# Kernel tuning notes

Hardware: AMD Instinct MI355X
Metric: run time of the kernel (lower is better)

The kernel has to match this reference:

```python
import jax, jax.numpy as jnp
import numpy as np
import math

B, T, D = 2, 2048, 1024
H, NL, DF = 16, 6, 4096
HD = D // H
EPS = 1e-5

def layer_norm(x, w, b):
    mu = jnp.mean(x, axis=-1, keepdims=True)
    var = jnp.mean((x - mu) ** 2, axis=-1, keepdims=True)
    return (x - mu) * jax.lax.rsqrt(var + EPS) * w + b

def setup_inputs() -> dict:
    key = jax.random.key(0)
    ks = jax.random.split(key, 12)
    def w(k, shape, scale=0.02):
        return jax.random.normal(k, shape, dtype=jnp.float32) * scale
    inp = {
        'sequences': jax.random.normal(ks[0], (B, T, D), dtype=jnp.float32),
        'Wq': w(ks[1], (NL, D, D)), 'bq': jnp.zeros((NL, D), jnp.float32),
        'Wk': w(ks[2], (NL, D, D)), 'bk': jnp.zeros((NL, D), jnp.float32),
        'Wv': w(ks[3], (NL, D, D)), 'bv': jnp.zeros((NL, D), jnp.float32),
        'Wo': w(ks[4], (NL, D, D)), 'bo': jnp.zeros((NL, D), jnp.float32),
        'Wz': w(ks[5], (NL, D, D)), 'bz': jnp.zeros((NL, D), jnp.float32),
        'Wr': w(ks[6], (NL, D, D)), 'br': jnp.zeros((NL, D), jnp.float32),
        'W1': w(ks[7], (NL, D, DF)), 'b1': jnp.zeros((NL, DF), jnp.float32),
        'W2': w(ks[8], (NL, DF, D)), 'b2': jnp.zeros((NL, D), jnp.float32),
        'ln1_w': jnp.ones((NL, D), jnp.float32), 'ln1_b': jnp.zeros((NL, D), jnp.float32),
        'ln2_w': jnp.ones((NL, D), jnp.float32), 'ln2_b': jnp.zeros((NL, D), jnp.float32),
        'lnf_w': jnp.ones((D,), jnp.float32), 'lnf_b': jnp.zeros((D,), jnp.float32),
    }
    return inp

def reference(sequences, Wq, bq, Wk, bk, Wv, bv, Wo, bo, Wz, bz, Wr, br,
              W1, b1, W2, b2, ln1_w, ln1_b, ln2_w, ln2_b, lnf_w, lnf_b):
    scale = 1.0 / math.sqrt(HD)
    causal = jnp.tril(jnp.ones((T, T), dtype=bool))  # mask[L:L+T, :L+T] with L=0
    x = sequences
    src = x
    for i in range(NL):
        xn = layer_norm(x, ln1_w[i], ln1_b[i])
        # QKV -> [B, H, T, HD]
        q = (xn @ Wq[i] + bq[i]).reshape(B, T, H, HD).transpose(0, 2, 1, 3)
        k = (xn @ Wk[i] + bk[i]).reshape(B, T, H, HD).transpose(0, 2, 1, 3)
        v = (xn @ Wv[i] + bv[i]).reshape(B, T, H, HD).transpose(0, 2, 1, 3)
        att = jnp.einsum('bhqd,bhkd->bhqk', q, k) * scale
        att = jnp.where(causal, att, -jnp.inf)
        att = jax.nn.softmax(att, axis=-1)
        y = jnp.einsum('bhqk,bhkd->bhqd', att, v)
        y = y.transpose(0, 2, 1, 3).reshape(B, T, D)
        x_attn = y @ Wo[i] + bo[i]
        z = jax.nn.sigmoid(xn @ Wz[i] + bz[i])
        r = jax.nn.sigmoid(xn @ Wr[i] + br[i])
        h_tilde = jnp.tanh(r * x_attn)
        x = (1.0 - z) * x + z * h_tilde
        xm = layer_norm(x, ln2_w[i], ln2_b[i])
        mlp = jax.nn.gelu(xm @ W1[i] + b1[i], approximate=False) @ W2[i] + b2[i]
        x = (1.0 - z) * x + z * mlp
        x = x + src
    x = layer_norm(x, lnf_w, lnf_b)
    return x
```

## Files before the change

### kernel.cpp

```cpp
#include <hip/hip_runtime.h>
#include <hip/hip_bf16.h>
#include <math.h>

#define B_ 2
#define T_ 2048
#define D_ 1024
#define H_ 16
#define NL_ 6
#define DF_ 4096
#define HD_ 64
#define M_ (B_*T_)

typedef __bf16 bf16;
typedef __attribute__((ext_vector_type(8))) __bf16 bf16x8;
typedef __attribute__((ext_vector_type(4))) float f32x4;
typedef __attribute__((ext_vector_type(16))) float f32x16;
typedef __attribute__((ext_vector_type(4))) unsigned u32x4;

#define BAR() __builtin_amdgcn_s_barrier()
#define LGKM0() asm volatile("s_waitcnt lgkmcnt(0)" ::: "memory")
#define VMC(n) asm volatile("s_waitcnt vmcnt(" #n ")" ::: "memory")

__device__ __forceinline__ void gload_lds16(const void* g, void* l) {
    __builtin_amdgcn_global_load_lds((const __attribute__((address_space(1))) void*)g,
                                     (__attribute__((address_space(3))) void*)l, 16, 0, 0);
}

__device__ __forceinline__ unsigned pk2(float a, float b) {
    bf16 lo = (bf16)a, hb = (bf16)b;
    return (unsigned)__builtin_bit_cast(unsigned short, lo) |
           ((unsigned)__builtin_bit_cast(unsigned short, hb) << 16);
}

template<bool OUT_BF16>
__global__ __launch_bounds__(256) void ln_kernel(const float* __restrict__ x,
        const float* __restrict__ w, const float* __restrict__ b,
        void* __restrict__ out) {
    const int row = blockIdx.x;
    const int t = threadIdx.x;
    const float4 xv = *(const float4*)(x + (long)row * D_ + t * 4);
    float s  = xv.x + xv.y + xv.z + xv.w;
    float sq = xv.x*xv.x + xv.y*xv.y + xv.z*xv.z + xv.w*xv.w;
    #pragma unroll
    for (int m = 32; m; m >>= 1) { s += __shfl_xor(s, m); sq += __shfl_xor(sq, m); }
    __shared__ float red[8];
    const int wid = t >> 6, lid = t & 63;
    if (lid == 0) { red[wid] = s; red[wid + 4] = sq; }
    __syncthreads();
    s  = red[0] + red[1] + red[2] + red[3];
    sq = red[4] + red[5] + red[6] + red[7];
    const float mu   = s * (1.0f / D_);
    const float var  = sq * (1.0f / D_) - mu * mu;
    const float rstd = rsqrtf(var + 1e-5f);
    const float4 wv = *(const float4*)(w + t * 4);
    const float4 bv = *(const float4*)(b + t * 4);
    float o0 = (xv.x - mu) * rstd * wv.x + bv.x;
    float o1 = (xv.y - mu) * rstd * wv.y + bv.y;
    float o2 = (xv.z - mu) * rstd * wv.z + bv.z;
    float o3 = (xv.w - mu) * rstd * wv.w + bv.w;
    if (OUT_BF16) {
        bf16* o = (bf16*)out + (long)row * D_ + t * 4;
        o[0] = (bf16)o0; o[1] = (bf16)o1; o[2] = (bf16)o2; o[3] = (bf16)o3;
    } else {
        float* o = (float*)out + (long)row * D_ + t * 4;
        o[0] = o0; o[1] = o1; o[2] = o2; o[3] = o3;
    }
}

__global__ __launch_bounds__(256) void wconv_all(
        const float* __restrict__ Wq, const float* __restrict__ Wk,
        const float* __restrict__ Wv, const float* __restrict__ Wz,
        const float* __restrict__ Wr, const float* __restrict__ Wo,
        const float* __restrict__ W1, const float* __restrict__ W2,
        bf16* __restrict__ wt) {
    __shared__ float s[32][33];
    const int bid = blockIdx.x;
    const float* src; bf16* dst; int t, K, nlg;
    if (bid < 6144) {
        const int m = bid >> 10; t = bid & 1023; K = 1024; nlg = 5;
        switch (m) {
            case 0: src = Wq; dst = wt; break;
            case 1: src = Wk; dst = wt + (1u << 20); break;
            case 2: src = Wv; dst = wt + (2u << 20); break;
            case 3: src = Wz; dst = wt + (3u << 20); break;
            case 4: src = Wr; dst = wt + (4u << 20); break;
            default: src = Wo; dst = wt + (5u << 20); break;
        }
    } else if (bid < 10240) {
        t = bid - 6144; K = 1024; nlg = 7; src = W1; dst = wt + (6u << 20);
    } else {
        t = bid - 10240; K = 4096; nlg = 5; src = W2; dst = wt + (10u << 20);
    }
    const int N = 1 << (nlg + 5);
    const int k0 = (t >> nlg) * 32, n0 = (t & ((1 << nlg) - 1)) * 32;
    const int c = threadIdx.x & 31, r8 = threadIdx.x >> 5;
    #pragma unroll
    for (int it = 0; it < 4; it++)
        s[r8 + it*8][c] = src[(long)(k0 + r8 + it*8) * N + n0 + c];
    __syncthreads();
    #pragma unroll
    for (int it = 0; it < 4; it++)
        dst[(long)(n0 + r8 + it*8) * K + k0 + c] = (bf16)s[c][r8 + it*8];
}

#define MFMA16(a, b, c) __builtin_amdgcn_mfma_f32_16x16x32_bf16(a, b, c, 0, 0, 0)

__device__ __forceinline__ void gemm256_core(const bf16* __restrict__ A, const bf16* __restrict__ Bt,
        const int Ks, const int NT, const int m0, const int n0, char* lds, f32x4 (&acc)[8][4]) {
    const int tid = threadIdx.x;
    const int lane = tid & 63, w = tid >> 6;
    const int wm = w >> 2, wn = w & 3;
    const int cl = lane & 15, gl = lane >> 4;
    const int srow = lane >> 3;
    const int scol = ((lane & 7) ^ srow) * 8;
    const bf16* pa0 = A  + (size_t)(m0 + w * 16 + srow) * Ks + scol;
    const bf16* pa1 = pa0 + (size_t)8 * Ks;
    const bf16* pb0 = Bt + (size_t)(n0 + w * 16 + srow) * Ks + scol;
    const bf16* pb1 = pb0 + (size_t)8 * Ks;
    char* la = lds + w * 2048;
    char* lb = lds + 65536 + w * 2048;
    const size_t hA = (size_t)128 * Ks;

#define STGA(H, KT, BUF) do { \
    gload_lds16(pa0 + (size_t)(H) * hA + (size_t)(KT) * 64, la + (BUF) * 32768 + (H) * 16384); \
    gload_lds16(pa1 + (size_t)(H) * hA + (size_t)(KT) * 64, la + (BUF) * 32768 + (H) * 16384 + 1024); } while (0)
#define STGB(H, KT, BUF) do { \
    gload_lds16(pb0 + (size_t)(H) * hA + (size_t)(KT) * 64, lb + (BUF) * 32768 + (H) * 16384); \
    gload_lds16(pb1 + (size_t)(H) * hA + (size_t)(KT) * 64, lb + (BUF) * 32768 + (H) * 16384 + 1024); } while (0)

    STGA(0, 0, 0); STGA(1, 0, 0); STGB(0, 0, 0); STGB(1, 0, 0);
    STGB(0, 1, 1); STGA(0, 1, 1); STGA(1, 1, 1);
    VMC(6);
    BAR();

    const int X0  = (gl * 16) ^ ((cl & 7) << 4);
    const int rdA = (wm * 128 + cl) * 128 + X0;
    const int rdB = (wn * 64  + cl) * 128 + X0;

    for (int kt = 0; kt < NT; ++kt) {
        const int buf = kt & 1;
        const char* sAb = lds + buf * 32768;
        const char* sBb = lds + 65536 + buf * 32768;
        const bool st1 = (kt + 1 < NT), st2 = (kt + 2 < NT);
        bf16x8 a0[4][2], a4[4][2], b01[2][2], b23[2][2];
        #pragma unroll
        for (int mi = 0; mi < 4; mi++) {
            a0[mi][0] = *(const bf16x8*)(sAb + rdA + mi * 2048);
            a0[mi][1] = *(const bf16x8*)(sAb + (rdA ^ 64) + mi * 2048);
        }
        #pragma unroll
        for (int ni = 0; ni < 2; ni++) {
            b01[ni][0] = *(const bf16x8*)(sBb + rdB + ni * 2048);
            b01[ni][1] = *(const bf16x8*)(sBb + (rdB ^ 64) + ni * 2048);
        }
        if (st1) STGB(1, kt + 1, buf ^ 1);
        BAR(); LGKM0();
        __builtin_amdgcn_s_setprio(1);
        #pragma unroll
        for (int mi = 0; mi < 4; mi++)
            #pragma unroll
            for (int ni = 0; ni < 2; ni++) {
                acc[mi][ni] = MFMA16(a0[mi][0], b01[ni][0], acc[mi][ni]);
                acc[mi][ni] = MFMA16(a0[mi][1], b01[ni][1], acc[mi][ni]);
            }
        __builtin_amdgcn_s_setprio(0);
        BAR();
        #pragma unroll
        for (int mi = 0; mi < 4; mi++) {
            a4[mi][0] = *(const bf16x8*)(sAb + rdA + (mi + 4) * 2048);
            a4[mi][1] = *(const bf16x8*)(sAb + (rdA ^ 64) + (mi + 4) * 2048);
        }
        BAR(); LGKM0();
        __builtin_amdgcn_s_setprio(1);
        #pragma unroll
        for (int mi = 0; mi < 4; mi++)
            #pragma unroll
            for (int ni = 0; ni < 2; ni++) {
                acc[mi + 4][ni] = MFMA16(a4[mi][0], b01[ni][0], acc[mi + 4][ni]);
                acc[mi + 4][ni] = MFMA16(a4[mi][1], b01[ni][1], acc[mi + 4][ni]);
            }
        __builtin_amdgcn_s_setprio(0);
        BAR();
        #pragma unroll
        for (int ni = 0; ni < 2; ni++) {
            b23[ni][0] = *(const bf16x8*)(sBb + rdB + (ni + 2) * 2048);
            b23[ni][1] = *(const bf16x8*)(sBb + (rdB ^ 64) + (ni + 2) * 2048);
        }
        if (st2) STGA(0, kt + 2, buf);
        BAR(); LGKM0();
        __builtin_amdgcn_s_setprio(1);
        #pragma unroll
        for (int mi = 0; mi < 4; mi++)
            #pragma unroll
            for (int ni = 0; ni < 2; ni++) {
                acc[mi + 4][ni + 2] = MFMA16(a4[mi][0], b23[ni][0], acc[mi + 4][ni + 2]);
                acc[mi + 4][ni + 2] = MFMA16(a4[mi][1], b23[ni][1], acc[mi + 4][ni + 2]);
            }
        __builtin_amdgcn_s_setprio(0);
        BAR();
        if (st2) { STGA(1, kt + 2, buf); STGB(0, kt + 2, buf); }
        __builtin_amdgcn_s_setprio(1);
        #pragma unroll
        for (int mi = 0; mi < 4; mi++)
            #pragma unroll
            for (int ni = 0; ni < 2; ni++) {
                acc[mi][ni + 2] = MFMA16(a0[mi][0], b23[ni][0], acc[mi][ni + 2]);
                acc[mi][ni + 2] = MFMA16(a0[mi][1], b23[ni][1], acc[mi][ni + 2]);
            }
        __builtin_amdgcn_s_setprio(0);
        if (st2)      { VMC(6); }
        else if (st1) { VMC(0); }
        BAR();
    }
#undef STGA
#undef STGB
}

__global__ __launch_bounds__(512, 2) void gemm5_256(const bf16* __restrict__ A, const bf16* __restrict__ Bt,
        const float* __restrict__ bq, const float* __restrict__ bk, const float* __restrict__ bvv,
        const float* __restrict__ bz, const float* __restrict__ br,
        bf16* __restrict__ oq, bf16* __restrict__ ok, bf16* __restrict__ ov,
        float* __restrict__ oz, float* __restrict__ orr) {
    __shared__ __align__(16) char lds[131072];
    int bid = blockIdx.x;
    bid = (bid & 7) * 40 + (bid >> 3);
    const int m0 = (bid / 20) * 256, n0 = (bid % 20) * 256;
    f32x4 acc[8][4];
    #pragma unroll
    for (int i = 0; i < 8; i++)
        #pragma unroll
        for (int j = 0; j < 4; j++) acc[i][j] = (f32x4){0.f, 0.f, 0.f, 0.f};
    gemm256_core(A, Bt, 1024, 16, m0, n0, lds, acc);
    const int tid = threadIdx.x, lane = tid & 63, w = tid >> 6;
    const int wm = w >> 2, wn = w & 3, cl = lane & 15, gl = lane >> 4;
    const int seg = n0 >> 10;
    const int lc0 = (n0 & 1023) + wn * 64;
    const float* bias; int mode; void* outp;
    switch (seg) {
        case 0:  bias = bq;  mode = 0; outp = oq;  break;
        case 1:  bias = bk;  mode = 0; outp = ok;  break;
        case 2:  bias = bvv; mode = 1; outp = ov;  break;
        case 3:  bias = bz;  mode = 2; outp = oz;  break;
        default: bias = br;  mode = 2; outp = orr; break;
    }
    #pragma unroll
    for (int mi = 0; mi < 8; mi++) {
        #pragma unroll
        for (int ni = 0; ni < 4; ni++) {
            const int lcol = lc0 + ni * 16 + cl;
            const float bv = bias[lcol];
            #pragma unroll
            for (int r = 0; r < 4; r++) {
                const int row = m0 + wm * 128 + mi * 16 + gl * 4 + r;
                const float v = acc[mi][ni][r] + bv;
                if (mode == 0) {
                    ((bf16*)outp)[(long)row * 1024 + lcol] = (bf16)v;
                } else if (mode == 1) {
                    ((bf16*)outp)[((long)(row >> 11) * 1024 + lcol) * T_ + (row & 2047)] = (bf16)v;
                } else {
                    ((float*)outp)[(long)row * 1024 + lcol] = 1.0f / (1.0f + __expf(-v));
                }
            }
        }
    }
}

__global__ __launch_bounds__(512, 2) void gemmG_256(const bf16* __restrict__ A, const bf16* __restrict__ Bt,
        const float* __restrict__ bias, bf16* __restrict__ out) {
    __shared__ __align__(16) char lds[131072];
    int bid = blockIdx.x;
    bid = (bid & 7) * 32 + (bid >> 3);
    const int m0 = (bid >> 4) * 256, n0 = (bid & 15) * 256;
    f32x4 acc[8][4];
    #pragma unroll
    for (int i = 0; i < 8; i++)
        #pragma unroll
        for (int j = 0; j < 4; j++) acc[i][j] = (f32x4){0.f, 0.f, 0.f, 0.f};
    gemm256_core(A, Bt, 1024, 16, m0, n0, lds, acc);
    const int tid = threadIdx.x, lane = tid & 63, w = tid >> 6;
    const int wm = w >> 2, wn = w & 3, cl = lane & 15, gl = lane >> 4;
    #pragma unroll
    for (int mi = 0; mi < 8; mi++) {
        #pragma unroll
        for (int ni = 0; ni < 4; ni++) {
            const int col = n0 + wn * 64 + ni * 16 + cl;
            const float bv = bias[col];
            #pragma unroll
            for (int r = 0; r < 4; r++) {
                const int row = m0 + wm * 128 + mi * 16 + gl * 4 + r;
                float v = acc[mi][ni][r] + bv;
                v = 0.5f * v * (1.0f + erff(v * 0.70710678118f));
                out[(long)row * DF_ + col] = (bf16)v;
            }
        }
    }
}

__global__ __launch_bounds__(512, 2) void gemmP_256(const bf16* __restrict__ A, const bf16* __restrict__ Bt,
        float* __restrict__ p0, float* __restrict__ p1, float* __restrict__ p2, float* __restrict__ p3) {
    __shared__ __align__(16) char lds[131072];
    int bid = blockIdx.x;
    bid = (bid & 7) * 32 + (bid >> 3);
    const int mt = bid >> 4, rest = bid & 15;
    const int nt = rest >> 2, s = rest & 3;
    const int m0 = mt * 256, n0 = nt * 256;
    f32x4 acc[8][4];
    #pragma unroll
    for (int i = 0; i < 8; i++)
        #pragma unroll
        for (int j = 0; j < 4; j++) acc[i][j] = (f32x4){0.f, 0.f, 0.f, 0.f};
    gemm256_core(A + s * 1024, Bt + s * 1024, 4096, 16, m0, n0, lds, acc);
    float* outp = (s == 0) ? p0 : (s == 1) ? p1 : (s == 2) ? p2 : p3;
    const int tid = threadIdx.x, lane = tid & 63, w = tid >> 6;
    const int wm = w >> 2, wn = w & 3, cl = lane & 15, gl = lane >> 4;
    #pragma unroll
    for (int mi = 0; mi < 8; mi++) {
        #pragma unroll
        for (int ni = 0; ni < 4; ni++) {
            const int col = n0 + wn * 64 + ni * 16 + cl;
            #pragma unroll
            for (int r = 0; r < 4; r++) {
                const int row = m0 + wm * 128 + mi * 16 + gl * 4 + r;
                outp[(long)row * 1024 + col] = acc[mi][ni][r];
            }
        }
    }
}

__global__ __launch_bounds__(256) void gemmWo_kernel(const bf16* __restrict__ A,
        const bf16* __restrict__ Bt, const float* __restrict__ bias,
        float* __restrict__ out) {
    __shared__ bf16 sA[128 * 32];
    __shared__ bf16 sB[128 * 32];
    const int tid = threadIdx.x;
    int bid = blockIdx.x;
    bid = (bid & 7) * 32 + (bid >> 3);
    const int m0 = (bid >> 3) * 128, n0 = (bid & 7) * 128;
    f32x4 acc[4][4];
    #pragma unroll
    for (int i = 0; i < 4; i++)
        #pragma unroll
        for (int j = 0; j < 4; j++) acc[i][j] = (f32x4){0.f, 0.f, 0.f, 0.f};
    const int lane = tid & 63, w = tid >> 6;
    const int wr = (w >> 1) * 64, wc = (w & 1) * 64;
    const int cl = lane & 15, gl = lane >> 4;
    const int srow = tid >> 2, skoff = (tid & 3) * 8;
    const bf16* ga = A  + (long)(m0 + srow) * D_ + skoff;
    const bf16* gb = Bt + (long)(n0 + srow) * D_ + skoff;
    char* sAc = (char*)sA;
    char* sBc = (char*)sB;
    const int wb = w * 1024;
    for (int k0 = 0; k0 < D_; k0 += 32) {
        if (k0) __syncthreads();
        gload_lds16(ga + k0,            sAc + wb);
        gload_lds16(ga + 64 * D_ + k0,  sAc + 4096 + wb);
        gload_lds16(gb + k0,            sBc + wb);
        gload_lds16(gb + 64 * D_ + k0,  sBc + 4096 + wb);
        __syncthreads();
        bf16x8 af[4], bfr[4];
        #pragma unroll
        for (int i = 0; i < 4; i++) af[i]  = *(const bf16x8*)(sA + (wr + i*16 + cl) * 32 + 8 * gl);
        #pragma unroll
        for (int j = 0; j < 4; j++) bfr[j] = *(const bf16x8*)(sB + (wc + j*16 + cl) * 32 + 8 * gl);
        #pragma unroll
        for (int i = 0; i < 4; i++)
            #pragma unroll
            for (int j = 0; j < 4; j++)
                acc[i][j] = MFMA16(af[i], bfr[j], acc[i][j]);
    }
    #pragma unroll
    for (int i = 0; i < 4; i++) {
        #pragma unroll
        for (int j = 0; j < 4; j++) {
            const int gcol = n0 + wc + j * 16 + cl;
            const float bv = bias[gcol];
            #pragma unroll
            for (int r = 0; r < 4; r++) {
                const int grow = m0 + wr + i * 16 + gl * 4 + r;
                out[(long)grow * D_ + gcol] = acc[i][j][r] + bv;
            }
        }
    }
}

#define LOADKV(K0,K1,K2,K3,V00,V01,V10,V11,KVB) do { \
    const long kro_ = (long)((KVB) + col) * D_ + 8 * hi; \
    K0 = *(const bf16x8*)(kB + kro_); \
    K1 = *(const bf16x8*)(kB + kro_ + 16); \
    K2 = *(const bf16x8*)(kB + kro_ + 32); \
    K3 = *(const bf16x8*)(kB + kro_ + 48); \
    const long vro_ = (long)col * T_ + (KVB) + 8 * hi; \
    V00 = *(const bf16x8*)(vB + vro_); \
    V10 = *(const bf16x8*)(vB + vro_ + 16); \
    V01 = *(const bf16x8*)(vB + vro_ + (long)32 * T_); \
    V11 = *(const bf16x8*)(vB + vro_ + (long)32 * T_ + 16); \
} while (0)

#define PROC(K0,K1,K2,K3,V00,V01,V10,V11,JJ) do { \
    f32x16 S; \
    _Pragma("unroll") for (int i_ = 0; i_ < 16; i_++) S[i_] = 0.f; \
    S = __builtin_amdgcn_mfma_f32_32x32x16_bf16(K0, qf0, S, 0, 0, 0); \
    S = __builtin_amdgcn_mfma_f32_32x32x16_bf16(K1, qf1, S, 0, 0, 0); \
    S = __builtin_amdgcn_mfma_f32_32x32x16_bf16(K2, qf2, S, 0, 0, 0); \
    S = __builtin_amdgcn_mfma_f32_32x32x16_bf16(K3, qf3, S, 0, 0, 0); \
    float p_[16]; \
    const bool dg_ = (JJ) == nt - 1; \
    _Pragma("unroll") for (int r_ = 0; r_ < 16; r_++) { \
        p_[r_] = S[r_] * 0.125f; \
        const int kvl_ = (r_ & 3) + 8 * (r_ >> 2) + 4 * hi; \
        if (dg_ && kvl_ > col) p_[r_] = -3.0e38f; \
    } \
    float tm_ = p_[0]; \
    _Pragma("unroll") for (int r_ = 1; r_ < 16; r_++) tm_ = fmaxf(tm_, p_[r_]); \
    tm_ = fmaxf(tm_, __shfl_xor(tm_, 32)); \
    const float mn_ = fmaxf(mrun, tm_); \
    const float al_ = __expf(mrun - mn_); \
    mrun = mn_; \
    float ts_ = 0.f; \
    _Pragma("unroll") for (int r_ = 0; r_ < 16; r_++) { p_[r_] = __expf(p_[r_] - mn_); ts_ += p_[r_]; } \
    ts_ += __shfl_xor(ts_, 32); \
    lrun = lrun * al_ + ts_; \
    _Pragma("unroll") for (int i_ = 0; i_ < 16; i_++) { Od0[i_] *= al_; Od1[i_] *= al_; } \
    const unsigned w0_ = pk2(p_[0],  p_[1]),  w1_ = pk2(p_[2],  p_[3]); \
    const unsigned w2_ = pk2(p_[4],  p_[5]),  w3_ = pk2(p_[6],  p_[7]); \
    const unsigned w4_ = pk2(p_[8],  p_[9]),  w5_ = pk2(p_[10], p_[11]); \
    const unsigned w6_ = pk2(p_[12], p_[13]), w7_ = pk2(p_[14], p_[15]); \
    const unsigned x0_ = __shfl_xor((int)w0_, 32), x1_ = __shfl_xor((int)w1_, 32); \
    const unsigned x2_ = __shfl_xor((int)w2_, 32), x3_ = __shfl_xor((int)w3_, 32); \
    const unsigned x4_ = __shfl_xor((int)w4_, 32), x5_ = __shfl_xor((int)w5_, 32); \
    const unsigned x6_ = __shfl_xor((int)w6_, 32), x7_ = __shfl_xor((int)w7_, 32); \
    const u32x4 c0_ = hi ? (u32x4){x2_, x3_, w2_, w3_} : (u32x4){w0_, w1_, x0_, x1_}; \
    const u32x4 c1_ = hi ? (u32x4){x6_, x7_, w6_, w7_} : (u32x4){w4_, w5_, x4_, x5_}; \
    const bf16x8 pb0_ = __builtin_bit_cast(bf16x8, c0_); \
    const bf16x8 pb1_ = __builtin_bit_cast(bf16x8, c1_); \
    Od0 = __builtin_amdgcn_mfma_f32_32x32x16_bf16(V00, pb0_, Od0, 0, 0, 0); \
    Od0 = __builtin_amdgcn_mfma_f32_32x32x16_bf16(V10, pb1_, Od0, 0, 0, 0); \
    Od1 = __builtin_amdgcn_mfma_f32_32x32x16_bf16(V01, pb0_, Od1, 0, 0, 0); \
    Od1 = __builtin_amdgcn_mfma_f32_32x32x16_bf16(V11, pb1_, Od1, 0, 0, 0); \
} while (0)

__global__ __launch_bounds__(128) void attn_kernel(const bf16* __restrict__ q,
        const bf16* __restrict__ k, const bf16* __restrict__ vT,
        bf16* __restrict__ y) {
    const int tid = threadIdx.x, wid = tid >> 6, lane = tid & 63;
    const int col = lane & 31, hi = lane >> 5;
    const int bid = blockIdx.x;
    const int xcd = bid & 7, idx = bid >> 3;
    const int bh = xcd + 8 * (idx & 3);
    const int g = idx >> 2;
    const int qt = wid ? (63 - g) : g;
    const int qb = qt * 32;
    const int b = bh >> 4, h = bh & 15;

    const bf16* qB = q  + (long)b * T_ * D_ + h * HD_;
    const bf16* kB = k  + (long)b * T_ * D_ + h * HD_;
    const bf16* vB = vT + (long)b * D_ * T_ + (long)h * HD_ * T_;

    bf16x8 qf0, qf1, qf2, qf3;
    {
        const long qo = (long)(qb + col) * D_ + 8 * hi;
        qf0 = *(const bf16x8*)(qB + qo);
        qf1 = *(const bf16x8*)(qB + qo + 16);
        qf2 = *(const bf16x8*)(qB + qo + 32);
        qf3 = *(const bf16x8*)(qB + qo + 48);
    }

    f32x16 Od0, Od1;
    #pragma unroll
    for (int i = 0; i < 16; i++) { Od0[i] = 0.f; Od1[i] = 0.f; }
    float mrun = -INFINITY, lrun = 0.f;

    bf16x8 ka0, ka1, ka2, ka3, va00, va01, va10, va11;
    bf16x8 kb0, kb1, kb2, kb3, vb00, vb01, vb10, vb11;
    const int nt = qt + 1;

    int jj = 0;
    LOADKV(ka0, ka1, ka2, ka3, va00, va01, va10, va11, 0);
    while (true) {
        if (jj + 1 < nt) LOADKV(kb0, kb1, kb2, kb3, vb00, vb01, vb10, vb11, (jj + 1) * 32);
        PROC(ka0, ka1, ka2, ka3, va00, va01, va10, va11, jj);
        if (++jj >= nt) break;
        if (jj + 1 < nt) LOADKV(ka0, ka1, ka2, ka3, va00, va01, va10, va11, (jj + 1) * 32);
        PROC(kb0, kb1, kb2, kb3, vb00, vb01, vb10, vb11, jj);
        if (++jj >= nt) break;
    }

    const float inv = 1.0f / lrun;
    bf16* yr = y + (long)(b * T_ + qb + col) * D_ + h * HD_;
    #pragma unroll
    for (int rg = 0; rg < 4; rg++) {
        const int d0 = 8 * rg + 4 * hi;
        uint2 s0 = { pk2(Od0[4*rg] * inv, Od0[4*rg+1] * inv), pk2(Od0[4*rg+2] * inv, Od0[4*rg+3] * inv) };
        *(uint2*)(yr + d0) = s0;
        uint2 s1 = { pk2(Od1[4*rg] * inv, Od1[4*rg+1] * inv), pk2(Od1[4*rg+2] * inv, Od1[4*rg+3] * inv) };
        *(uint2*)(yr + 32 + d0) = s1;
    }
}

__global__ __launch_bounds__(256) void gate1_kernel(float* __restrict__ x,
        const float* __restrict__ z, const float* __restrict__ r,
        const float* __restrict__ xa) {
    const long i = ((long)blockIdx.x * 256 + threadIdx.x) * 4;
    float4 xv = *(const float4*)(x + i);
    const float4 zv = *(const float4*)(z + i);
    const float4 rv = *(const float4*)(r + i);
    const float4 av = *(const float4*)(xa + i);
    xv.x = (1.f - zv.x) * xv.x + zv.x * tanhf(rv.x * av.x);
    xv.y = (1.f - zv.y) * xv.y + zv.y * tanhf(rv.y * av.y);
    xv.z = (1.f - zv.z) * xv.z + zv.z * tanhf(rv.z * av.z);
    xv.w = (1.f - zv.w) * xv.w + zv.w * tanhf(rv.w * av.w);
    *(float4*)(x + i) = xv;
}

__global__ __launch_bounds__(256) void gate2_kernel(float* __restrict__ x,
        const float* __restrict__ z,
        const float* __restrict__ p0, const float* __restrict__ p1,
        const float* __restrict__ p2, const float* __restrict__ p3,
        const float* __restrict__ src, const float* __restrict__ b2) {
    const long i = ((long)blockIdx.x * 256 + threadIdx.x) * 4;
    float4 xv = *(const float4*)(x + i);
    const float4 zv = *(const float4*)(z + i);
    const float4 a0 = *(const float4*)(p0 + i);
    const float4 a1 = *(const float4*)(p1 + i);
    const float4 a2 = *(const float4*)(p2 + i);
    const float4 a3 = *(const float4*)(p3 + i);
    const float4 sv = *(const float4*)(src + i);
    const float4 bb = *(const float4*)(b2 + (i & 1023));
    const float mx = a0.x + a1.x + a2.x + a3.x + bb.x;
    const float my = a0.y + a1.y + a2.y + a3.y + bb.y;
    const float mz = a0.z + a1.z + a2.z + a3.z + bb.z;
    const float mw = a0.w + a1.w + a2.w + a3.w + bb.w;
    xv.x = (1.f - zv.x) * xv.x + zv.x * mx + sv.x;
    xv.y = (1.f - zv.y) * xv.y + zv.y * my + sv.y;
    xv.z = (1.f - zv.z) * xv.z + zv.z * mz + sv.z;
    xv.w = (1.f - zv.w) * xv.w + zv.w * mw + sv.w;
    *(float4*)(x + i) = xv;
}

extern "C" void kernel_launch(void* const* d_in, const int* in_sizes, int n_in,
                              void* d_out, int out_size, void* d_ws, size_t ws_size,
                              hipStream_t stream) {
    const float* seq   = (const float*)d_in[0];
    const float* Wq    = (const float*)d_in[1];  const float* bq = (const float*)d_in[2];
    const float* Wk    = (const float*)d_in[3];  const float* bk = (const float*)d_in[4];
    const float* Wv    = (const float*)d_in[5];  const float* bv = (const float*)d_in[6];
    const float* Wo    = (const float*)d_in[7];  const float* bo = (const float*)d_in[8];
    const float* Wz    = (const float*)d_in[9];  const float* bz = (const float*)d_in[10];
    const float* Wr    = (const float*)d_in[11]; const float* br = (const float*)d_in[12];
    const float* W1    = (const float*)d_in[13]; const float* b1 = (const float*)d_in[14];
    const float* W2    = (const float*)d_in[15]; const float* b2 = (const float*)d_in[16];
    const float* ln1w  = (const float*)d_in[17]; const float* ln1b = (const float*)d_in[18];
    const float* ln2w  = (const float*)d_in[19]; const float* ln2b = (const float*)d_in[20];
    const float* lnfw  = (const float*)d_in[21]; const float* lnfb = (const float*)d_in[22];

    char* ws = (char*)d_ws;
    float* x   = (float*)(ws);
    float* z   = (float*)(ws + ((size_t)16 << 20));
    float* r   = (float*)(ws + ((size_t)32 << 20));
    float* xa  = (float*)(ws + ((size_t)48 << 20));
    bf16*  xn  = (bf16*)(ws + ((size_t)64 << 20));
    bf16*  qb_ = (bf16*)(ws + ((size_t)72 << 20));
    bf16*  kb_ = (bf16*)(ws + ((size_t)80 << 20));
    bf16*  vtb = (bf16*)(ws + ((size_t)88 << 20));
    bf16*  yb  = (bf16*)(ws + ((size_t)96 << 20));
    bf16*  h1  = (bf16*)(ws + ((size_t)104 << 20));
    bf16*  wt  = (bf16*)(ws + ((size_t)136 << 20));
    float* pt2 = (float*)(ws + ((size_t)172 << 20));
    float* pt3 = (float*)(ws + ((size_t)188 << 20));

    bf16* wto = wt + (5u << 20);
    bf16* wt1 = wt + (6u << 20);
    bf16* wt2 = wt + (10u << 20);

    hipMemcpyAsync(x, seq, (size_t)M_ * D_ * 4, hipMemcpyDeviceToDevice, stream);

    for (int i = 0; i < NL_; i++) {
        const long dd = (long)i * D_ * D_;
        wconv_all<<<14336, 256, 0, stream>>>(Wq + dd, Wk + dd, Wv + dd, Wz + dd,
                                             Wr + dd, Wo + dd,
                                             W1 + (long)i * D_ * DF_,
                                             W2 + (long)i * DF_ * D_, wt);
        ln_kernel<true><<<M_, 256, 0, stream>>>(x, ln1w + i * D_, ln1b + i * D_, xn);
        gemm5_256<<<320, 512, 0, stream>>>(xn, wt,
                bq + i * D_, bk + i * D_, bv + i * D_, bz + i * D_, br + i * D_,
                qb_, kb_, vtb, z, r);
        attn_kernel<<<1024, 128, 0, stream>>>(qb_, kb_, vtb, yb);
        gemmWo_kernel<<<256, 256, 0, stream>>>(yb, wto, bo + i * D_, xa);
        gate1_kernel<<<(M_ * D_) / 1024, 256, 0, stream>>>(x, z, r, xa);
        ln_kernel<true><<<M_, 256, 0, stream>>>(x, ln2w + i * D_, ln2b + i * D_, xn);
        gemmG_256<<<256, 512, 0, stream>>>(xn, wt1, b1 + i * DF_, h1);
        gemmP_256<<<256, 512, 0, stream>>>(h1, wt2, xa, r, pt2, pt3);
        gate2_kernel<<<(M_ * D_) / 1024, 256, 0, stream>>>(x, z, xa, r, pt2, pt3, seq, b2 + i * D_);
    }
    ln_kernel<false><<<M_, 256, 0, stream>>>(x, lnfw, lnfb, d_out);
}
```

Baseline: 1.969 ms.

## Replace 256x256 GEMM tiles with 256x128 tiles and BK=32 for higher occupancy

Rewrites the shared GEMM core from a 256x256 output tile with K-step 64 into a 256x128 tile with K-step 32, using a simpler two-phase MFMA loop and a new LDS swizzle. LDS use drops from 128KB to 48KB, and launch bounds now allow 4 blocks per CU. Grid sizes double for the QKV/gate, FFN1 and FFN2 GEMMs to cover the smaller tiles. The goal is more resident blocks and better load balance across CUs. In exchange, each tile has lower arithmetic intensity and there are more barriers per unit of K.

```diff
diff --git a/kernel.cpp b/kernel.cpp
--- a/kernel.cpp
+++ b/kernel.cpp
@@ -105,134 +105,83 @@
 
 #define MFMA16(a, b, c) __builtin_amdgcn_mfma_f32_16x16x32_bf16(a, b, c, 0, 0, 0)
 
-__device__ __forceinline__ void gemm256_core(const bf16* __restrict__ A, const bf16* __restrict__ Bt,
-        const int Ks, const int NT, const int m0, const int n0, char* lds, f32x4 (&acc)[8][4]) {
+__device__ __forceinline__ void gemm128_core(const bf16* __restrict__ A, const bf16* __restrict__ Bt,
+        const int Ks, const int NT, const int m0, const int n0, char* lds, f32x4 (&acc)[4][4]) {
     const int tid = threadIdx.x;
     const int lane = tid & 63, w = tid >> 6;
-    const int wm = w >> 2, wn = w & 3;
+    const int wm = w >> 1, wn = w & 1;
     const int cl = lane & 15, gl = lane >> 4;
-    const int srow = lane >> 3;
-    const int scol = ((lane & 7) ^ srow) * 8;
-    const bf16* pa0 = A  + (size_t)(m0 + w * 16 + srow) * Ks + scol;
-    const bf16* pa1 = pa0 + (size_t)8 * Ks;
-    const bf16* pb0 = Bt + (size_t)(n0 + w * 16 + srow) * Ks + scol;
-    const bf16* pb1 = pb0 + (size_t)8 * Ks;
-    char* la = lds + w * 2048;
-    char* lb = lds + 65536 + w * 2048;
-    const size_t hA = (size_t)128 * Ks;
-
-#define STGA(H, KT, BUF) do { \
-    gload_lds16(pa0 + (size_t)(H) * hA + (size_t)(KT) * 64, la + (BUF) * 32768 + (H) * 16384); \
-    gload_lds16(pa1 + (size_t)(H) * hA + (size_t)(KT) * 64, la + (BUF) * 32768 + (H) * 16384 + 1024); } while (0)
-#define STGB(H, KT, BUF) do { \
-    gload_lds16(pb0 + (size_t)(H) * hA + (size_t)(KT) * 64, lb + (BUF) * 32768 + (H) * 16384); \
-    gload_lds16(pb1 + (size_t)(H) * hA + (size_t)(KT) * 64, lb + (BUF) * 32768 + (H) * 16384 + 1024); } while (0)
-
-    STGA(0, 0, 0); STGA(1, 0, 0); STGB(0, 0, 0); STGB(1, 0, 0);
-    STGB(0, 1, 1); STGA(0, 1, 1); STGA(1, 1, 1);
-    VMC(6);
+    const int srow = lane >> 2;
+    const int sxc = (((lane & 3) ^ (srow & 3)) << 3);
+    const bf16* pa0 = A  + (size_t)(m0 + w * 32 + srow) * Ks + sxc;
+    const bf16* pa1 = pa0 + (size_t)16 * Ks;
+    const bf16* pb  = Bt + (size_t)(n0 + w * 16 + srow) * Ks + sxc;
+    char* laA = lds + w * 2048;
+    char* laB = lds + 32768 + w * 1024;
+
+#define STG(KT, BUF) do { \
+    gload_lds16(pa0 + (size_t)(KT) * 32, laA + (BUF) * 16384); \
+    gload_lds16(pa1 + (size_t)(KT) * 32, laA + (BUF) * 16384 + 1024); \
+    gload_lds16(pb  + (size_t)(KT) * 32, laB + (BUF) * 8192); } while (0)
+
+    STG(0, 0); STG(1, 1);
+    VMC(3);
     BAR();
 
-    const int X0  = (gl * 16) ^ ((cl & 7) << 4);
-    const int rdA = (wm * 128 + cl) * 128 + X0;
-    const int rdB = (wn * 64  + cl) * 128 + X0;
+    const int xo  = ((gl ^ (cl & 3)) << 4);
+    const int rdA = (wm * 64 + cl) * 64 + xo;
+    const int rdB = (wn * 64 + cl) * 64 + xo;
 
     for (int kt = 0; kt < NT; ++kt) {
         const int buf = kt & 1;
-        const char* sAb = lds + buf * 32768;
-        const char* sBb = lds + 65536 + buf * 32768;
-        const bool st1 = (kt + 1 < NT), st2 = (kt + 2 < NT);
-        bf16x8 a0[4][2], a4[4][2], b01[2][2], b23[2][2];
-        #pragma unroll
-        for (int mi = 0; mi < 4; mi++) {
-            a0[mi][0] = *(const bf16x8*)(sAb + rdA + mi * 2048);
-            a0[mi][1] = *(const bf16x8*)(sAb + (rdA ^ 64) + mi * 2048);
-        }
-        #pragma unroll
-        for (int ni = 0; ni < 2; ni++) {
-            b01[ni][0] = *(const bf16x8*)(sBb + rdB + ni * 2048);
-            b01[ni][1] = *(const bf16x8*)(sBb + (rdB ^ 64) + ni * 2048);
-        }
-        if (st1) STGB(1, kt + 1, buf ^ 1);
+        const char* sA = lds + buf * 16384;
+        const char* sB = lds + 32768 + buf * 8192;
+        bf16x8 a[4], b[4];
+        #pragma unroll
+        for (int mi = 0; mi < 4; mi++) a[mi] = *(const bf16x8*)(sA + rdA + mi * 1024);
+        #pragma unroll
+        for (int ni = 0; ni < 4; ni++) b[ni] = *(const bf16x8*)(sB + rdB + ni * 1024);
         BAR(); LGKM0();
         __builtin_amdgcn_s_setprio(1);
         #pragma unroll
-        for (int mi = 0; mi < 4; mi++)
-            #pragma unroll
-            for (int ni = 0; ni < 2; ni++) {
-                acc[mi][ni] = MFMA16(a0[mi][0], b01[ni][0], acc[mi][ni]);
-                acc[mi][ni] = MFMA16(a0[mi][1], b01[ni][1], acc[mi][ni]);
-            }
+        for (int mi = 0; mi < 2; mi++)
+            #pragma unroll
+            for (int ni = 0; ni < 4; ni++)
+                acc[mi][ni] = MFMA16(a[mi], b[ni], acc[mi][ni]);
         __builtin_amdgcn_s_setprio(0);
         BAR();
-        #pragma unroll
-        for (int mi = 0; mi < 4; mi++) {
-            a4[mi][0] = *(const bf16x8*)(sAb + rdA + (mi + 4) * 2048);
-            a4[mi][1] = *(const bf16x8*)(sAb + (rdA ^ 64) + (mi + 4) * 2048);
-        }
-        BAR(); LGKM0();
+        if (kt + 2 < NT) STG(kt + 2, buf);
         __builtin_amdgcn_s_setprio(1);
         #pragma unroll
-        for (int mi = 0; mi < 4; mi++)
-            #pragma unroll
-            for (int ni = 0; ni < 2; ni++) {
-                acc[mi + 4][ni] = MFMA16(a4[mi][0], b01[ni][0], acc[mi + 4][ni]);
-                acc[mi + 4][ni] = MFMA16(a4[mi][1], b01[ni][1], acc[mi + 4][ni]);
-            }
+        for (int mi = 2; mi < 4; mi++)
+            #pragma unroll
+            for (int ni = 0; ni < 4; ni++)
+                acc[mi][ni] = MFMA16(a[mi], b[ni], acc[mi][ni]);
         __builtin_amdgcn_s_setprio(0);
+        if (kt + 2 < NT)      { VMC(3); }
+        else if (kt + 1 < NT) { VMC(0); }
         BAR();
-        #pragma unroll
-        for (int ni = 0; ni < 2; ni++) {
-            b23[ni][0] = *(const bf16x8*)(sBb + rdB + (ni + 2) * 2048);
-            b23[ni][1] = *(const bf16x8*)(sBb + (rdB ^ 64) + (ni + 2) * 2048);
-        }
-        if (st2) STGA(0, kt + 2, buf);
-        BAR(); LGKM0();
-        __builtin_amdgcn_s_setprio(1);
-        #pragma unroll
-        for (int mi = 0; mi < 4; mi++)
-            #pragma unroll
-            for (int ni = 0; ni < 2; ni++) {
-                acc[mi + 4][ni + 2] = MFMA16(a4[mi][0], b23[ni][0], acc[mi + 4][ni + 2]);
-                acc[mi + 4][ni + 2] = MFMA16(a4[mi][1], b23[ni][1], acc[mi + 4][ni + 2]);
-            }
-        __builtin_amdgcn_s_setprio(0);
-        BAR();
-        if (st2) { STGA(1, kt + 2, buf); STGB(0, kt + 2, buf); }
-        __builtin_amdgcn_s_setprio(1);
-        #pragma unroll
-        for (int mi = 0; mi < 4; mi++)
-            #pragma unroll
-            for (int ni = 0; ni < 2; ni++) {
-                acc[mi][ni + 2] = MFMA16(a0[mi][0], b23[ni][0], acc[mi][ni + 2]);
-                acc[mi][ni + 2] = MFMA16(a0[mi][1], b23[ni][1], acc[mi][ni + 2]);
-            }
-        __builtin_amdgcn_s_setprio(0);
-        if (st2)      { VMC(6); }
-        else if (st1) { VMC(0); }
-        BAR();
-    }
-#undef STGA
-#undef STGB
-}
-
-__global__ __launch_bounds__(512, 2) void gemm5_256(const bf16* __restrict__ A, const bf16* __restrict__ Bt,
+    }
+#undef STG
+}
+
+__global__ __launch_bounds__(512, 4) void gemm5_k(const bf16* __restrict__ A, const bf16* __restrict__ Bt,
         const float* __restrict__ bq, const float* __restrict__ bk, const float* __restrict__ bvv,
         const float* __restrict__ bz, const float* __restrict__ br,
         bf16* __restrict__ oq, bf16* __restrict__ ok, bf16* __restrict__ ov,
         float* __restrict__ oz, float* __restrict__ orr) {
-    __shared__ __align__(16) char lds[131072];
+    __shared__ __align__(16) char lds[49152];
     int bid = blockIdx.x;
-    bid = (bid & 7) * 40 + (bid >> 3);
-    const int m0 = (bid / 20) * 256, n0 = (bid % 20) * 256;
-    f32x4 acc[8][4];
-    #pragma unroll
-    for (int i = 0; i < 8; i++)
+    bid = (bid & 7) * 80 + (bid >> 3);
+    const int m0 = (bid / 40) * 256, n0 = (bid % 40) * 128;
+    f32x4 acc[4][4];
+    #pragma unroll
+    for (int i = 0; i < 4; i++)
         #pragma unroll
         for (int j = 0; j < 4; j++) acc[i][j] = (f32x4){0.f, 0.f, 0.f, 0.f};
-    gemm256_core(A, Bt, 1024, 16, m0, n0, lds, acc);
+    gemm128_core(A, Bt, 1024, 32, m0, n0, lds, acc);
     const int tid = threadIdx.x, lane = tid & 63, w = tid >> 6;
-    const int wm = w >> 2, wn = w & 3, cl = lane & 15, gl = lane >> 4;
+    const int wm = w >> 1, wn = w & 1, cl = lane & 15, gl = lane >> 4;
     const int seg = n0 >> 10;
     const int lc0 = (n0 & 1023) + wn * 64;
     const float* bias; int mode; void* outp;
@@ -244,14 +193,14 @@
         default: bias = br;  mode = 2; outp = orr; break;
     }
     #pragma unroll
-    for (int mi = 0; mi < 8; mi++) {
+    for (int mi = 0; mi < 4; mi++) {
         #pragma unroll
         for (int ni = 0; ni < 4; ni++) {
             const int lcol = lc0 + ni * 16 + cl;
             const float bv = bias[lcol];
             #pragma unroll
             for (int r = 0; r < 4; r++) {
-                const int row = m0 + wm * 128 + mi * 16 + gl * 4 + r;
+                const int row = m0 + wm * 64 + mi * 16 + gl * 4 + r;
                 const float v = acc[mi][ni][r] + bv;
                 if (mode == 0) {
                     ((bf16*)outp)[(long)row * 1024 + lcol] = (bf16)v;
@@ -265,29 +214,29 @@
     }
 }
 
-__global__ __launch_bounds__(512, 2) void gemmG_256(const bf16* __restrict__ A, const bf16* __restrict__ Bt,
+__global__ __launch_bounds__(512, 4) void gemmG_k(const bf16* __restrict__ A, const bf16* __restrict__ Bt,
         const float* __restrict__ bias, bf16* __restrict__ out) {
-    __shared__ __align__(16) char lds[131072];
+    __shared__ __align__(16) char lds[49152];
     int bid = blockIdx.x;
-    bid = (bid & 7) * 32 + (bid >> 3);
-    const int m0 = (bid >> 4) * 256, n0 = (bid & 15) * 256;
-    f32x4 acc[8][4];
-    #pragma unroll
-    for (int i = 0; i < 8; i++)
+    bid = (bid & 7) * 64 + (bid >> 3);
+    const int m0 = (bid >> 5) * 256, n0 = (bid & 31) * 128;
+    f32x4 acc[4][4];
+    #pragma unroll
+    for (int i = 0; i < 4; i++)
         #pragma unroll
         for (int j = 0; j < 4; j++) acc[i][j] = (f32x4){0.f, 0.f, 0.f, 0.f};
-    gemm256_core(A, Bt, 1024, 16, m0, n0, lds, acc);
+    gemm128_core(A, Bt, 1024, 32, m0, n0, lds, acc);
     const int tid = threadIdx.x, lane = tid & 63, w = tid >> 6;
-    const int wm = w >> 2, wn = w & 3, cl = lane & 15, gl = lane >> 4;
-    #pragma unroll
-    for (int mi = 0; mi < 8; mi++) {
+    const int wm = w >> 1, wn = w & 1, cl = lane & 15, gl = lane >> 4;
+    #pragma unroll
+    for (int mi = 0; mi < 4; mi++) {
         #pragma unroll
         for (int ni = 0; ni < 4; ni++) {
             const int col = n0 + wn * 64 + ni * 16 + cl;
             const float bv = bias[col];
             #pragma unroll
             for (int r = 0; r < 4; r++) {
-                const int row = m0 + wm * 128 + mi * 16 + gl * 4 + r;
+                const int row = m0 + wm * 64 + mi * 16 + gl * 4 + r;
                 float v = acc[mi][ni][r] + bv;
                 v = 0.5f * v * (1.0f + erff(v * 0.70710678118f));
                 out[(long)row * DF_ + col] = (bf16)v;
@@ -296,31 +245,30 @@
     }
 }
 
-__global__ __launch_bounds__(512, 2) void gemmP_256(const bf16* __restrict__ A, const bf16* __restrict__ Bt,
+__global__ __launch_bounds__(512, 4) void gemmP_k(const bf16* __restrict__ A, const bf16* __restrict__ Bt,
         float* __restrict__ p0, float* __restrict__ p1, float* __restrict__ p2, float* __restrict__ p3) {
-    __shared__ __align__(16) char lds[131072];
+    __shared__ __align__(16) char lds[49152];
     int bid = blockIdx.x;
-    bid = (bid & 7) * 32 + (bid >> 3);
-    const int mt = bid >> 4, rest = bid & 15;
-    const int nt = rest >> 2, s = rest & 3;
-    const int m0 = mt * 256, n0 = nt * 256;
-    f32x4 acc[8][4];
-    #pragma unroll
-    for (int i = 0; i < 8; i++)
+    bid = (bid & 7) * 64 + (bid >> 3);
+    const int mt = bid >> 5, s = (bid >> 3) & 3, ntl = bid & 7;
+    const int m0 = mt * 256, n0 = ntl * 128;
+    f32x4 acc[4][4];
+    #pragma unroll
+    for (int i = 0; i < 4; i++)
         #pragma unroll
         for (int j = 0; j < 4; j++) acc[i][j] = (f32x4){0.f, 0.f, 0.f, 0.f};
-    gemm256_core(A + s * 1024, Bt + s * 1024, 4096, 16, m0, n0, lds, acc);
+    gemm128_core(A + s * 1024, Bt + s * 1024, 4096, 32, m0, n0, lds, acc);
     float* outp = (s == 0) ? p0 : (s == 1) ? p1 : (s == 2) ? p2 : p3;
     const int tid = threadIdx.x, lane = tid & 63, w = tid >> 6;
-    const int wm = w >> 2, wn = w & 3, cl = lane & 15, gl = lane >> 4;
-    #pragma unroll
-    for (int mi = 0; mi < 8; mi++) {
+    const int wm = w >> 1, wn = w & 1, cl = lane & 15, gl = lane >> 4;
+    #pragma unroll
+    for (int mi = 0; mi < 4; mi++) {
         #pragma unroll
         for (int ni = 0; ni < 4; ni++) {
             const int col = n0 + wn * 64 + ni * 16 + cl;
             #pragma unroll
             for (int r = 0; r < 4; r++) {
-                const int row = m0 + wm * 128 + mi * 16 + gl * 4 + r;
+                const int row = m0 + wm * 64 + mi * 16 + gl * 4 + r;
                 outp[(long)row * 1024 + col] = acc[mi][ni][r];
             }
         }
@@ -581,15 +529,15 @@
                                              W1 + (long)i * D_ * DF_,
                                              W2 + (long)i * DF_ * D_, wt);
         ln_kernel<true><<<M_, 256, 0, stream>>>(x, ln1w + i * D_, ln1b + i * D_, xn);
-        gemm5_256<<<320, 512, 0, stream>>>(xn, wt,
+        gemm5_k<<<640, 512, 0, stream>>>(xn, wt,
                 bq + i * D_, bk + i * D_, bv + i * D_, bz + i * D_, br + i * D_,
                 qb_, kb_, vtb, z, r);
         attn_kernel<<<1024, 128, 0, stream>>>(qb_, kb_, vtb, yb);
         gemmWo_kernel<<<256, 256, 0, stream>>>(yb, wto, bo + i * D_, xa);
         gate1_kernel<<<(M_ * D_) / 1024, 256, 0, stream>>>(x, z, r, xa);
         ln_kernel<true><<<M_, 256, 0, stream>>>(x, ln2w + i * D_, ln2b + i * D_, xn);
-        gemmG_256<<<256, 512, 0, stream>>>(xn, wt1, b1 + i * DF_, h1);
-        gemmP_256<<<256, 512, 0, stream>>>(h1, wt2, xa, r, pt2, pt3);
+        gemmG_k<<<512, 512, 0, stream>>>(xn, wt1, b1 + i * DF_, h1);
+        gemmP_k<<<512, 512, 0, stream>>>(h1, wt2, xa, r, pt2, pt3);
         gate2_kernel<<<(M_ * D_) / 1024, 256, 0, stream>>>(x, z, xa, r, pt2, pt3, seq, b2 + i * D_);
     }
     ln_kernel<false><<<M_, 256, 0, stream>>>(x, lnfw, lnfb, d_out);
```

Measured after the change: 1.933 ms. No clear change (-1.8%).
